# Kernel tuning notes

Measured on AMD Instinct MI355X. Metric: run time of the kernel, lower is better.

Reference implementation:

```python
import jax, jax.numpy as jnp
import numpy as np

IN_F, OUT_F, GROUP, KROT, PACK, BATCH = 4096, 14336, 128, 8, 8, 16


def _pack_nibbles(nib):
    # nib: int32 in [0,16) with shape [R, C]; pack 8 consecutive cols into one int32
    shifts = 4 * jnp.arange(PACK, dtype=jnp.int32)
    return jnp.sum(nib.reshape(nib.shape[0], -1, PACK) << shifts, axis=-1).astype(jnp.int32)


def setup_inputs() -> dict:
    key = jax.random.key(0)
    ks = jax.random.split(key, 7)
    n_groups = IN_F // GROUP
    x = jax.random.normal(ks[0], (BATCH, IN_F), dtype=jnp.float16)
    theta = (0.1 * jax.random.normal(ks[1], (KROT, IN_F // 2), dtype=jnp.float32)).astype(jnp.float16)
    # each rotation round pairs channels via a permutation: (pairs[k,2i], pairs[k,2i+1])
    pairs = jnp.stack([
        jax.random.permutation(jax.random.fold_in(ks[2], k), IN_F)
        for k in range(KROT)
    ]).astype(jnp.int32)
    channel_scales = (1.0 + 0.01 * jax.random.normal(ks[3], (1, IN_F), dtype=jnp.float32)).astype(jnp.float16)
    qweight = _pack_nibbles(jax.random.randint(ks[4], (IN_F, OUT_F), 0, 16, dtype=jnp.int32))
    qzeros = _pack_nibbles(jax.random.randint(ks[5], (n_groups, OUT_F), 0, 16, dtype=jnp.int32))
    scales = (0.001 + 0.01 * jax.random.uniform(ks[6], (n_groups, OUT_F), dtype=jnp.float32)).astype(jnp.float16)
    return {"x": x, "theta": theta, "pairs": pairs, "channel_scales": channel_scales,
            "qweight": qweight, "qzeros": qzeros, "scales": scales}


def _rotate(x, theta, pairs, channel_scales):
    # KROT rounds of pairwise Givens rotations, then per-channel scaling
    cos = jnp.cos(theta.astype(jnp.float32)).astype(x.dtype)  # [KROT, IN/2]
    sin = jnp.sin(theta.astype(jnp.float32)).astype(x.dtype)
    for k in range(theta.shape[0]):
        ia, ib = pairs[k, 0::2], pairs[k, 1::2]
        a, b = x[..., ia], x[..., ib]
        x = x.at[..., ia].set(cos[k] * a - sin[k] * b).at[..., ib].set(sin[k] * a + cos[k] * b)
    return x * channel_scales


def _dequant(qweight, qzeros, scales, group_size, dtype):
    shifts = 4 * jnp.arange(PACK, dtype=jnp.int32)
    iw = ((qweight[:, :, None] >> shifts) & 0xF).reshape(qweight.shape[0], -1)  # [IN, OUT]
    iz = ((qzeros[:, :, None] >> shifts) & 0xF).reshape(qzeros.shape[0], -1)    # [n_groups, OUT]
    w = (iw - jnp.repeat(iz, group_size, axis=0)).astype(dtype)
    return w * jnp.repeat(scales, group_size, axis=0)


def reference(x, theta, pairs, channel_scales, qweight, qzeros, scales):
    group_size = x.shape[-1] // qzeros.shape[0]
    xr = _rotate(x, theta, pairs, channel_scales)
    w = _dequant(qweight, qzeros, scales, group_size, xr.dtype)  # [IN, OUT] fp16
    return xr @ w  # [BATCH, OUT]
```

## Files before the change

### kernel.cpp

```cpp
#include <hip/hip_runtime.h>
#include <cstdint>

#define IN_F   4096
#define OUT_F  14336
#define GROUP  128
#define KROT   8
#define BATCH  16
#define NJP    1792
#define NG     32

typedef __attribute__((ext_vector_type(8))) short short8;
typedef __attribute__((ext_vector_type(4))) float f32x4;

__device__ uint32_t g_xa[BATCH * IN_F / 2];
__device__ float    g_rs[NG * BATCH];
__device__ float    g_part[4 * BATCH * OUT_F];

static __device__ __forceinline__ unsigned short f2bf(float f) {
    union { float f; uint32_t i; } v; v.f = f;
    uint32_t u = v.i;
    uint32_t r = u + 0x7FFFu + ((u >> 16) & 1u);
    return (unsigned short)(r >> 16);
}
static __device__ __forceinline__ float bf2f(uint32_t u16) {
    union { uint32_t i; float f; } v; v.i = u16 << 16; return v.f;
}

__global__ __launch_bounds__(1024) void k_rotate(
    const float* __restrict__ x,
    const float* __restrict__ theta,
    const int*   __restrict__ pairs,
    const float* __restrict__ cscale)
{
    __shared__ float row[IN_F];
    const int b   = blockIdx.x;
    const int tid = threadIdx.x;

    int2  ij0[KROT], ij1[KROT];
    float c0[KROT], s0[KROT], c1[KROT], s1[KROT];
#pragma unroll
    for (int k = 0; k < KROT; ++k) {
        const int2*  pk = (const int2*)(pairs + k * IN_F);
        const float* tk = theta + k * (IN_F / 2);
        ij0[k] = pk[tid];
        ij1[k] = pk[tid + 1024];
        __sincosf(tk[tid],        &s0[k], &c0[k]);
        __sincosf(tk[tid + 1024], &s1[k], &c1[k]);
    }

    for (int i = tid; i < IN_F; i += 1024) row[i] = x[b * IN_F + i];
    __syncthreads();

#pragma unroll
    for (int k = 0; k < KROT; ++k) {
        float a0 = row[ij0[k].x], b0 = row[ij0[k].y];
        float a1 = row[ij1[k].x], b1 = row[ij1[k].y];
        row[ij0[k].x] = c0[k] * a0 - s0[k] * b0;
        row[ij0[k].y] = s0[k] * a0 + c0[k] * b0;
        row[ij1[k].x] = c1[k] * a1 - s1[k] * b1;
        row[ij1[k].y] = s1[k] * a1 + c1[k] * b1;
        __syncthreads();
    }

    float p0, p1;
    {
        int i = tid;
        uint32_t lo = f2bf(row[2 * i]     * cscale[2 * i]);
        uint32_t hi = f2bf(row[2 * i + 1] * cscale[2 * i + 1]);
        g_xa[b * (IN_F / 2) + i] = lo | (hi << 16);
        p0 = bf2f(lo) + bf2f(hi);
        i = tid + 1024;
        lo = f2bf(row[2 * i]     * cscale[2 * i]);
        hi = f2bf(row[2 * i + 1] * cscale[2 * i + 1]);
        g_xa[b * (IN_F / 2) + i] = lo | (hi << 16);
        p1 = bf2f(lo) + bf2f(hi);
    }
#pragma unroll
    for (int m = 1; m < 64; m <<= 1) {
        p0 += __shfl_xor(p0, m, 64);
        p1 += __shfl_xor(p1, m, 64);
    }
    if ((tid & 63) == 0) {
        const int w = tid >> 6;
        g_rs[w * BATCH + b]        = p0;
        g_rs[(16 + w) * BATCH + b] = p1;
    }
}

__global__ __launch_bounds__(256, 2) void k_gemm(
    const int*   __restrict__ qweight,
    const int*   __restrict__ qzeros,
    const float* __restrict__ scales)
{
    __shared__ uint4 ldsb[4 * 512];

    const int tid  = threadIdx.x;
    const int bn   = blockIdx.x % 112;
    const int bk   = blockIdx.x / 112;
    const int n0   = bn * 128;
    const int jp0  = bn * 16;
    const int w    = tid >> 6;
    const int lane = tid & 63;
    const int jp   = lane & 15;
    const int rr   = lane >> 4;
    const int mrow = lane & 15;
    const int quad = lane >> 4;

    uint4* ldsw = ldsb + w * 512;

    float sv[2][8], tv[2][8];
    f32x4 rsv[2];
    {
        const int sh = 4 * (mrow & 7);
#pragma unroll
        for (int gi = 0; gi < 2; ++gi) {
            const int gg = bk * 8 + w * 2 + gi;
            rsv[gi] = *(const f32x4*)(g_rs + gg * BATCH + quad * 4);
#pragma unroll
            for (int t = 0; t < 8; ++t) {
                const int col = n0 + t * 16 + mrow;
                const float s = scales[(size_t)gg * OUT_F + col];
                const float z = 128.0f +
                    (float)(((uint32_t)qzeros[gg * NJP + (col >> 3)] >> sh) & 15u);
                sv[gi][t] = s;
                tv[gi][t] = s * z;
            }
        }
    }

    f32x4 m[8];
#pragma unroll
    for (int t = 0; t < 8; ++t) m[t] = (f32x4){0.f, 0.f, 0.f, 0.f};

#pragma unroll
    for (int gi = 0; gi < 2; ++gi) {
        const int gg = bk * 8 + w * 2 + gi;

        f32x4 ga[8];
#pragma unroll
        for (int t = 0; t < 8; ++t) ga[t] = (f32x4){0.f, 0.f, 0.f, 0.f};

#pragma unroll
        for (int sc = 0; sc < 4; ++sc) {
            const int kr0 = gg * GROUP + sc * 32 + rr * 8;

            uint32_t wc[8];
#pragma unroll
            for (int i = 0; i < 8; ++i)
                wc[i] = (uint32_t)qweight[(size_t)(kr0 + i) * NJP + jp0 + jp];

            union { uint4 q; short8 s; } af;
            af.q = *(const uint4*)(g_xa + mrow * (IN_F / 2)
                                   + ((gg * GROUP + sc * 32) >> 1) + quad * 4);

#pragma unroll
            for (int cc = 0; cc < 8; ++cc) {
                const int c  = cc ^ (jp & 7);
                const int sh = 4 * c;
                uint4 cell;
                uint32_t pk[4];
#pragma unroll
                for (int h = 0; h < 4; ++h) {
                    uint32_t lo = (wc[2 * h]     >> sh) & 15u;
                    uint32_t hi = (wc[2 * h + 1] >> sh) & 15u;
                    pk[h] = 0x43004300u | lo | (hi << 16);
                }
                cell.x = pk[0]; cell.y = pk[1]; cell.z = pk[2]; cell.w = pk[3];
                ldsw[rr * 128 + jp * 8 + c] = cell;
            }

#pragma unroll
            for (int t = 0; t < 8; ++t) {
                union { uint4 q; short8 s; } bf;
                bf.q = ldsw[quad * 128 + t * 16 + mrow];
                ga[t] = __builtin_amdgcn_mfma_f32_16x16x32_bf16(af.s, bf.s, ga[t], 0, 0, 0);
            }
        }

#pragma unroll
        for (int t = 0; t < 8; ++t)
#pragma unroll
            for (int r = 0; r < 4; ++r)
                m[t][r] = fmaf(sv[gi][t], ga[t][r],
                               fmaf(-tv[gi][t], rsv[gi][r], m[t][r]));
    }

    float* fw = (float*)ldsb + w * 2048;
#pragma unroll
    for (int t = 0; t < 8; ++t)
#pragma unroll
        for (int r = 0; r < 4; ++r)
            fw[(quad * 4 + r) * 128 + t * 16 + mrow] = m[t][r];
    __syncthreads();

    const float* fb   = (const float*)ldsb;
    const int    colg = (tid & 31) * 4;
    const int    row  = tid >> 5;
    f32x4 sA = {0.f, 0.f, 0.f, 0.f}, sB = {0.f, 0.f, 0.f, 0.f};
#pragma unroll
    for (int ww = 0; ww < 4; ++ww) {
        sA += *(const f32x4*)(fb + ww * 2048 + row * 128 + colg);
        sB += *(const f32x4*)(fb + ww * 2048 + (row + 8) * 128 + colg);
    }
    float* pp = g_part + (size_t)bk * BATCH * OUT_F + n0 + colg;
    *(f32x4*)(pp + (size_t)row * OUT_F)       = sA;
    *(f32x4*)(pp + (size_t)(row + 8) * OUT_F) = sB;
}

__global__ __launch_bounds__(128) void k_reduce(float* __restrict__ out)
{
    const int t = blockIdx.x * 128 + threadIdx.x;
    const size_t j = (size_t)t * 4;
    float4 a = *(const float4*)(g_part + j);
    float4 b = *(const float4*)(g_part + (size_t)BATCH * OUT_F + j);
    float4 c = *(const float4*)(g_part + (size_t)2 * BATCH * OUT_F + j);
    float4 d = *(const float4*)(g_part + (size_t)3 * BATCH * OUT_F + j);
    float4 s;
    s.x = (a.x + b.x) + (c.x + d.x);
    s.y = (a.y + b.y) + (c.y + d.y);
    s.z = (a.z + b.z) + (c.z + d.z);
    s.w = (a.w + b.w) + (c.w + d.w);
    *(float4*)(out + j) = s;
}

extern "C" void kernel_launch(void* const* d_in, const int* in_sizes, int n_in,
                              void* d_out, int out_size, void* d_ws, size_t ws_size,
                              hipStream_t stream) {
    const float* x       = (const float*)d_in[0];
    const float* theta   = (const float*)d_in[1];
    const int*   pairs   = (const int*)d_in[2];
    const float* cscale  = (const float*)d_in[3];
    const int*   qweight = (const int*)d_in[4];
    const int*   qzeros  = (const int*)d_in[5];
    const float* scales  = (const float*)d_in[6];
    float*       out     = (float*)d_out;
    (void)d_ws; (void)ws_size;

    k_rotate<<<16, 1024, 0, stream>>>(x, theta, pairs, cscale);
    k_gemm<<<448, 256, 0, stream>>>(qweight, qzeros, scales);
    k_reduce<<<(BATCH * OUT_F) / (128 * 4), 128, 0, stream>>>(out);
}
```

Baseline: 102.6 us.

## Prefetch next weight slice in GEMM loop and fuse split-K reduction via semaphore

The GEMM main loop is flattened into eight steps, and each step loads the next step's packed weights and activation fragment into registers before dequantizing and running MFMAs on the current ones. This is meant to hide global load latency behind compute. The separate reduce kernel is removed. Instead the last of the four split-K blocks for each column tile, found with an atomic counter, sums the partials and writes the output. This saves one kernel launch and one pass over the partials, but costs more registers, which could hurt occupancy, and adds a threadfence and atomic per block.

```diff
diff --git a/kernel.cpp b/kernel.cpp
--- a/kernel.cpp
+++ b/kernel.cpp
@@ -15,6 +15,7 @@
 __device__ uint32_t g_xa[BATCH * IN_F / 2];
 __device__ float    g_rs[NG * BATCH];
 __device__ float    g_part[4 * BATCH * OUT_F];
+__device__ int      g_sem[112];
 
 static __device__ __forceinline__ unsigned short f2bf(float f) {
     union { float f; uint32_t i; } v; v.f = f;
@@ -35,6 +36,8 @@
     __shared__ float row[IN_F];
     const int b   = blockIdx.x;
     const int tid = threadIdx.x;
+
+    if (b == 0 && tid < 112) g_sem[tid] = 0;
 
     int2  ij0[KROT], ij1[KROT];
     float c0[KROT], s0[KROT], c1[KROT], s1[KROT];
@@ -90,9 +93,11 @@
 __global__ __launch_bounds__(256, 2) void k_gemm(
     const int*   __restrict__ qweight,
     const int*   __restrict__ qzeros,
-    const float* __restrict__ scales)
+    const float* __restrict__ scales,
+    float*       __restrict__ out)
 {
     __shared__ uint4 ldsb[4 * 512];
+    __shared__ int   s_last;
 
     const int tid  = threadIdx.x;
     const int bn   = blockIdx.x % 112;
@@ -128,61 +133,80 @@
         }
     }
 
-    f32x4 m[8];
-#pragma unroll
-    for (int t = 0; t < 8; ++t) m[t] = (f32x4){0.f, 0.f, 0.f, 0.f};
-
-#pragma unroll
-    for (int gi = 0; gi < 2; ++gi) {
-        const int gg = bk * 8 + w * 2 + gi;
-
-        f32x4 ga[8];
-#pragma unroll
-        for (int t = 0; t < 8; ++t) ga[t] = (f32x4){0.f, 0.f, 0.f, 0.f};
-
-#pragma unroll
-        for (int sc = 0; sc < 4; ++sc) {
-            const int kr0 = gg * GROUP + sc * 32 + rr * 8;
-
-            uint32_t wc[8];
+    f32x4 m[8], ga[8];
+#pragma unroll
+    for (int t = 0; t < 8; ++t) {
+        m[t]  = (f32x4){0.f, 0.f, 0.f, 0.f};
+        ga[t] = (f32x4){0.f, 0.f, 0.f, 0.f};
+    }
+
+    const int kbase0 = (bk * 8 + w * 2) * GROUP;
+
+    uint32_t wc[8];
+    uint4    ac;
+    {
+        const int kb = kbase0 + rr * 8;
+#pragma unroll
+        for (int i = 0; i < 8; ++i)
+            wc[i] = (uint32_t)qweight[(size_t)(kb + i) * NJP + jp0 + jp];
+        ac = *(const uint4*)(g_xa + mrow * (IN_F / 2) + (kbase0 >> 1) + quad * 4);
+    }
+
+#pragma unroll
+    for (int it = 0; it < 8; ++it) {
+        uint32_t wn[8];
+        uint4    an;
+        if (it < 7) {
+            const int kb1 = kbase0 + (it + 1) * 32 + rr * 8;
 #pragma unroll
             for (int i = 0; i < 8; ++i)
-                wc[i] = (uint32_t)qweight[(size_t)(kr0 + i) * NJP + jp0 + jp];
-
-            union { uint4 q; short8 s; } af;
-            af.q = *(const uint4*)(g_xa + mrow * (IN_F / 2)
-                                   + ((gg * GROUP + sc * 32) >> 1) + quad * 4);
-
-#pragma unroll
-            for (int cc = 0; cc < 8; ++cc) {
-                const int c  = cc ^ (jp & 7);
-                const int sh = 4 * c;
-                uint4 cell;
-                uint32_t pk[4];
-#pragma unroll
-                for (int h = 0; h < 4; ++h) {
-                    uint32_t lo = (wc[2 * h]     >> sh) & 15u;
-                    uint32_t hi = (wc[2 * h + 1] >> sh) & 15u;
-                    pk[h] = 0x43004300u | lo | (hi << 16);
-                }
-                cell.x = pk[0]; cell.y = pk[1]; cell.z = pk[2]; cell.w = pk[3];
-                ldsw[rr * 128 + jp * 8 + c] = cell;
+                wn[i] = (uint32_t)qweight[(size_t)(kb1 + i) * NJP + jp0 + jp];
+            an = *(const uint4*)(g_xa + mrow * (IN_F / 2)
+                                 + ((kbase0 + (it + 1) * 32) >> 1) + quad * 4);
+        }
+
+#pragma unroll
+        for (int cc = 0; cc < 8; ++cc) {
+            const int c  = cc ^ (jp & 7);
+            const int sh = 4 * c;
+            uint4 cell;
+            uint32_t pk[4];
+#pragma unroll
+            for (int h = 0; h < 4; ++h) {
+                uint32_t lo = (wc[2 * h]     >> sh) & 15u;
+                uint32_t hi = (wc[2 * h + 1] >> sh) & 15u;
+                pk[h] = 0x43004300u | lo | (hi << 16);
             }
-
+            cell.x = pk[0]; cell.y = pk[1]; cell.z = pk[2]; cell.w = pk[3];
+            ldsw[rr * 128 + jp * 8 + c] = cell;
+        }
+
+        union { uint4 q; short8 s; } af;
+        af.q = ac;
+#pragma unroll
+        for (int t = 0; t < 8; ++t) {
+            union { uint4 q; short8 s; } bf;
+            bf.q = ldsw[quad * 128 + t * 16 + mrow];
+            ga[t] = __builtin_amdgcn_mfma_f32_16x16x32_bf16(af.s, bf.s, ga[t], 0, 0, 0);
+        }
+
+        if ((it & 3) == 3) {
+            const int gi = it >> 2;
 #pragma unroll
             for (int t = 0; t < 8; ++t) {
-                union { uint4 q; short8 s; } bf;
-                bf.q = ldsw[quad * 128 + t * 16 + mrow];
-                ga[t] = __builtin_amdgcn_mfma_f32_16x16x32_bf16(af.s, bf.s, ga[t], 0, 0, 0);
+#pragma unroll
+                for (int r = 0; r < 4; ++r)
+                    m[t][r] = fmaf(sv[gi][t], ga[t][r],
+                                   fmaf(-tv[gi][t], rsv[gi][r], m[t][r]));
+                ga[t] = (f32x4){0.f, 0.f, 0.f, 0.f};
             }
         }
 
-#pragma unroll
-        for (int t = 0; t < 8; ++t)
-#pragma unroll
-            for (int r = 0; r < 4; ++r)
-                m[t][r] = fmaf(sv[gi][t], ga[t][r],
-                               fmaf(-tv[gi][t], rsv[gi][r], m[t][r]));
+        if (it < 7) {
+#pragma unroll
+            for (int i = 0; i < 8; ++i) wc[i] = wn[i];
+            ac = an;
+        }
     }
 
     float* fw = (float*)ldsb + w * 2048;
@@ -205,22 +229,30 @@
     float* pp = g_part + (size_t)bk * BATCH * OUT_F + n0 + colg;
     *(f32x4*)(pp + (size_t)row * OUT_F)       = sA;
     *(f32x4*)(pp + (size_t)(row + 8) * OUT_F) = sB;
-}
-
-__global__ __launch_bounds__(128) void k_reduce(float* __restrict__ out)
-{
-    const int t = blockIdx.x * 128 + threadIdx.x;
-    const size_t j = (size_t)t * 4;
-    float4 a = *(const float4*)(g_part + j);
-    float4 b = *(const float4*)(g_part + (size_t)BATCH * OUT_F + j);
-    float4 c = *(const float4*)(g_part + (size_t)2 * BATCH * OUT_F + j);
-    float4 d = *(const float4*)(g_part + (size_t)3 * BATCH * OUT_F + j);
-    float4 s;
-    s.x = (a.x + b.x) + (c.x + d.x);
-    s.y = (a.y + b.y) + (c.y + d.y);
-    s.z = (a.z + b.z) + (c.z + d.z);
-    s.w = (a.w + b.w) + (c.w + d.w);
-    *(float4*)(out + j) = s;
+
+    __threadfence();
+    __syncthreads();
+    if (tid == 0) {
+        int old = __hip_atomic_fetch_add(&g_sem[bn], 1, __ATOMIC_ACQ_REL,
+                                         __HIP_MEMORY_SCOPE_AGENT);
+        s_last = (old == 3);
+    }
+    __syncthreads();
+    if (s_last) {
+        __threadfence();
+        const int r2 = tid >> 4;
+        const int c2 = (tid & 15) * 8;
+        const size_t base = (size_t)r2 * OUT_F + n0 + c2;
+        f32x4 a0 = {0.f, 0.f, 0.f, 0.f}, a1 = {0.f, 0.f, 0.f, 0.f};
+#pragma unroll
+        for (int kc = 0; kc < 4; ++kc) {
+            const float* q = g_part + (size_t)kc * BATCH * OUT_F + base;
+            a0 += *(const f32x4*)(q);
+            a1 += *(const f32x4*)(q + 4);
+        }
+        *(f32x4*)(out + base)     = a0;
+        *(f32x4*)(out + base + 4) = a1;
+    }
 }
 
 extern "C" void kernel_launch(void* const* d_in, const int* in_sizes, int n_in,
@@ -237,6 +269,5 @@
     (void)d_ws; (void)ws_size;
 
     k_rotate<<<16, 1024, 0, stream>>>(x, theta, pairs, cscale);
-    k_gemm<<<448, 256, 0, stream>>>(qweight, qzeros, scales);
-    k_reduce<<<(BATCH * OUT_F) / (128 * 4), 128, 0, stream>>>(out);
-}
+    k_gemm<<<448, 256, 0, stream>>>(qweight, qzeros, scales, out);
+}
```

Result: slower. 162.2 us (+58.1%).

## Double split-K factor so each wave handles one quant group

Applied to the files above, without the earlier changes.

The GEMM grid is split into 8 K-chunks instead of 4, so each wave processes a single 128-row quantization group rather than two. The grid doubles to 896 blocks, launch bounds allow 4 blocks per CU, and the reduce kernel sums 8 partial buffers. The goal is more parallelism and better latency hiding for the memory-bound weight stream, at the cost of twice as much partial-sum traffic and a heavier reduce.

```diff
diff --git a/kernel.cpp b/kernel.cpp
--- a/kernel.cpp
+++ b/kernel.cpp
@@ -8,13 +8,14 @@
 #define BATCH  16
 #define NJP    1792
 #define NG     32
+#define NKC    8
 
 typedef __attribute__((ext_vector_type(8))) short short8;
 typedef __attribute__((ext_vector_type(4))) float f32x4;
 
 __device__ uint32_t g_xa[BATCH * IN_F / 2];
 __device__ float    g_rs[NG * BATCH];
-__device__ float    g_part[4 * BATCH * OUT_F];
+__device__ float    g_part[NKC * BATCH * OUT_F];
 
 static __device__ __forceinline__ unsigned short f2bf(float f) {
     union { float f; uint32_t i; } v; v.f = f;
@@ -87,7 +88,7 @@
     }
 }
 
-__global__ __launch_bounds__(256, 2) void k_gemm(
+__global__ __launch_bounds__(256, 4) void k_gemm(
     const int*   __restrict__ qweight,
     const int*   __restrict__ qzeros,
     const float* __restrict__ scales)
@@ -108,81 +109,64 @@
 
     uint4* ldsw = ldsb + w * 512;
 
-    float sv[2][8], tv[2][8];
-    f32x4 rsv[2];
+    const int gg     = bk * 4 + w;
+    const int kbase0 = gg * GROUP;
+
+    float sv[8], tv[8];
+    f32x4 rsv;
     {
         const int sh = 4 * (mrow & 7);
-#pragma unroll
-        for (int gi = 0; gi < 2; ++gi) {
-            const int gg = bk * 8 + w * 2 + gi;
-            rsv[gi] = *(const f32x4*)(g_rs + gg * BATCH + quad * 4);
-#pragma unroll
-            for (int t = 0; t < 8; ++t) {
-                const int col = n0 + t * 16 + mrow;
-                const float s = scales[(size_t)gg * OUT_F + col];
-                const float z = 128.0f +
-                    (float)(((uint32_t)qzeros[gg * NJP + (col >> 3)] >> sh) & 15u);
-                sv[gi][t] = s;
-                tv[gi][t] = s * z;
+        rsv = *(const f32x4*)(g_rs + gg * BATCH + quad * 4);
+#pragma unroll
+        for (int t = 0; t < 8; ++t) {
+            const int col = n0 + t * 16 + mrow;
+            const float s = scales[(size_t)gg * OUT_F + col];
+            const float z = 128.0f +
+                (float)(((uint32_t)qzeros[gg * NJP + (col >> 3)] >> sh) & 15u);
+            sv[t] = s;
+            tv[t] = s * z;
+        }
+    }
+
+    f32x4 ga[8];
+#pragma unroll
+    for (int t = 0; t < 8; ++t) ga[t] = (f32x4){0.f, 0.f, 0.f, 0.f};
+
+#pragma unroll
+    for (int it = 0; it < 4; ++it) {
+        const int kb = kbase0 + it * 32 + rr * 8;
+
+        uint32_t wc[8];
+#pragma unroll
+        for (int i = 0; i < 8; ++i)
+            wc[i] = (uint32_t)qweight[(size_t)(kb + i) * NJP + jp0 + jp];
+
+        union { uint4 q; short8 s; } af;
+        af.q = *(const uint4*)(g_xa + mrow * (IN_F / 2)
+                               + ((kbase0 + it * 32) >> 1) + quad * 4);
+
+#pragma unroll
+        for (int cc = 0; cc < 8; ++cc) {
+            const int c  = cc ^ (jp & 7);
+            const int sh = 4 * c;
+            uint4 cell;
+            uint32_t pk[4];
+#pragma unroll
+            for (int h = 0; h < 4; ++h) {
+                uint32_t lo = (wc[2 * h]     >> sh) & 15u;
+                uint32_t hi = (wc[2 * h + 1] >> sh) & 15u;
+                pk[h] = 0x43004300u | lo | (hi << 16);
             }
+            cell.x = pk[0]; cell.y = pk[1]; cell.z = pk[2]; cell.w = pk[3];
+            ldsw[rr * 128 + jp * 8 + c] = cell;
         }
-    }
-
-    f32x4 m[8];
-#pragma unroll
-    for (int t = 0; t < 8; ++t) m[t] = (f32x4){0.f, 0.f, 0.f, 0.f};
-
-#pragma unroll
-    for (int gi = 0; gi < 2; ++gi) {
-        const int gg = bk * 8 + w * 2 + gi;
-
-        f32x4 ga[8];
-#pragma unroll
-        for (int t = 0; t < 8; ++t) ga[t] = (f32x4){0.f, 0.f, 0.f, 0.f};
-
-#pragma unroll
-        for (int sc = 0; sc < 4; ++sc) {
-            const int kr0 = gg * GROUP + sc * 32 + rr * 8;
-
-            uint32_t wc[8];
-#pragma unroll
-            for (int i = 0; i < 8; ++i)
-                wc[i] = (uint32_t)qweight[(size_t)(kr0 + i) * NJP + jp0 + jp];
-
-            union { uint4 q; short8 s; } af;
-            af.q = *(const uint4*)(g_xa + mrow * (IN_F / 2)
-                                   + ((gg * GROUP + sc * 32) >> 1) + quad * 4);
-
-#pragma unroll
-            for (int cc = 0; cc < 8; ++cc) {
-                const int c  = cc ^ (jp & 7);
-                const int sh = 4 * c;
-                uint4 cell;
-                uint32_t pk[4];
-#pragma unroll
-                for (int h = 0; h < 4; ++h) {
-                    uint32_t lo = (wc[2 * h]     >> sh) & 15u;
-                    uint32_t hi = (wc[2 * h + 1] >> sh) & 15u;
-                    pk[h] = 0x43004300u | lo | (hi << 16);
-                }
-                cell.x = pk[0]; cell.y = pk[1]; cell.z = pk[2]; cell.w = pk[3];
-                ldsw[rr * 128 + jp * 8 + c] = cell;
-            }
-
-#pragma unroll
-            for (int t = 0; t < 8; ++t) {
-                union { uint4 q; short8 s; } bf;
-                bf.q = ldsw[quad * 128 + t * 16 + mrow];
-                ga[t] = __builtin_amdgcn_mfma_f32_16x16x32_bf16(af.s, bf.s, ga[t], 0, 0, 0);
-            }
+
+#pragma unroll
+        for (int t = 0; t < 8; ++t) {
+            union { uint4 q; short8 s; } bf;
+            bf.q = ldsw[quad * 128 + t * 16 + mrow];
+            ga[t] = __builtin_amdgcn_mfma_f32_16x16x32_bf16(af.s, bf.s, ga[t], 0, 0, 0);
         }
-
-#pragma unroll
-        for (int t = 0; t < 8; ++t)
-#pragma unroll
-            for (int r = 0; r < 4; ++r)
-                m[t][r] = fmaf(sv[gi][t], ga[t][r],
-                               fmaf(-tv[gi][t], rsv[gi][r], m[t][r]));
     }
 
     float* fw = (float*)ldsb + w * 2048;
@@ -190,7 +174,8 @@
     for (int t = 0; t < 8; ++t)
 #pragma unroll
         for (int r = 0; r < 4; ++r)
-            fw[(quad * 4 + r) * 128 + t * 16 + mrow] = m[t][r];
+            fw[(quad * 4 + r) * 128 + t * 16 + mrow] =
+                fmaf(sv[t], ga[t][r], -tv[t] * rsv[r]);
     __syncthreads();
 
     const float* fb   = (const float*)ldsb;
@@ -211,16 +196,11 @@
 {
     const int t = blockIdx.x * 128 + threadIdx.x;
     const size_t j = (size_t)t * 4;
-    float4 a = *(const float4*)(g_part + j);
-    float4 b = *(const float4*)(g_part + (size_t)BATCH * OUT_F + j);
-    float4 c = *(const float4*)(g_part + (size_t)2 * BATCH * OUT_F + j);
-    float4 d = *(const float4*)(g_part + (size_t)3 * BATCH * OUT_F + j);
-    float4 s;
-    s.x = (a.x + b.x) + (c.x + d.x);
-    s.y = (a.y + b.y) + (c.y + d.y);
-    s.z = (a.z + b.z) + (c.z + d.z);
-    s.w = (a.w + b.w) + (c.w + d.w);
-    *(float4*)(out + j) = s;
+    f32x4 s = {0.f, 0.f, 0.f, 0.f};
+#pragma unroll
+    for (int kc = 0; kc < NKC; ++kc)
+        s += *(const f32x4*)(g_part + (size_t)kc * BATCH * OUT_F + j);
+    *(f32x4*)(out + j) = s;
 }
 
 extern "C" void kernel_launch(void* const* d_in, const int* in_sizes, int n_in,
@@ -237,6 +217,6 @@
     (void)d_ws; (void)ws_size;
 
     k_rotate<<<16, 1024, 0, stream>>>(x, theta, pairs, cscale);
-    k_gemm<<<448, 256, 0, stream>>>(qweight, qzeros, scales);
+    k_gemm<<<112 * NKC, 256, 0, stream>>>(qweight, qzeros, scales);
     k_reduce<<<(BATCH * OUT_F) / (128 * 4), 128, 0, stream>>>(out);
 }
```

Result: no change. 104.0 us (+1.3%).
